# Kernel optimization log

Measured on AMD Instinct MI355X. Metric: run time of the kernel, lower is better.

The kernel has to match this reference:

```python
import jax, jax.numpy as jnp
import numpy as np

B, S, E = 2, 2049, 512
H, WIN = 8, 1024
D = E // H


def setup_inputs() -> dict:
    key = jax.random.key(0)
    ks = jax.random.split(key, 11)
    sc = 0.02
    return {
        "x": jax.random.normal(ks[0], (B, S, E), dtype=jnp.float32),
        "Wq": jax.random.normal(ks[1], (E, E), dtype=jnp.float32) * sc,
        "bq": jnp.zeros((E,), dtype=jnp.float32),
        "Wk": jax.random.normal(ks[2], (E, E), dtype=jnp.float32) * sc,
        "bk": jnp.zeros((E,), dtype=jnp.float32),
        "Wv": jax.random.normal(ks[3], (E, E), dtype=jnp.float32) * sc,
        "bv": jnp.zeros((E,), dtype=jnp.float32),
        "Wo": jax.random.normal(ks[4], (E, E), dtype=jnp.float32) * sc,
        "bo": jnp.zeros((E,), dtype=jnp.float32),
        "w_gate": jax.random.normal(ks[5], (2 * E,), dtype=jnp.float32) * sc,
        "b_gate": jnp.zeros((), dtype=jnp.float32),
    }


def reference(x, Wq, bq, Wk, bk, Wv, bv, Wo, bo, w_gate, b_gate):
    scale = D ** -0.5
    q_flat = x @ Wq + bq  # [B,S,E]
    k_flat = x @ Wk + bk
    v_flat = x @ Wv + bv
    q = q_flat.reshape(B, S, H, D).transpose(0, 2, 1, 3)  # [B,H,S,D]
    k = k_flat.reshape(B, S, H, D).transpose(0, 2, 1, 3)
    v = v_flat.reshape(B, S, H, D).transpose(0, 2, 1, 3)

    scores = jnp.einsum("bhqd,bhkd->bhqk", q, k) * scale  # [B,H,S,S]

    # Gaussian positional bias: -0.5*|i-j|^2/sigma^2, sigma = window/2
    pos = jnp.arange(S)
    dist = jnp.abs(pos[:, None] - pos[None, :]).astype(jnp.float32)
    sigma = WIN / 2.0
    bias = -0.5 * dist ** 2 / (sigma ** 2)  # [S,S]
    scores = scores + bias[None, None]

    # Pairwise gate: sigmoid(concat(q_i,k_j) @ w + b) == sigmoid(q_i.wq + k_j.wk + b)
    gq = q_flat @ w_gate[:E]       # [B,S]
    gk = k_flat @ w_gate[E:]       # [B,S]
    gates = jax.nn.sigmoid(gq[:, :, None] + gk[:, None, :] + b_gate)  # [B,S,S]
    scores = scores * gates[:, None]  # broadcast over heads

    local_mask = jnp.where(dist <= WIN, 0.0, -jnp.inf).astype(jnp.float32)
    scores = scores + local_mask[None, None]

    attn = jax.nn.softmax(scores, axis=-1)
    out = jnp.einsum("bhqk,bhkd->bhqd", attn, v)  # [B,H,S,D]
    out = out.transpose(0, 2, 1, 3).reshape(B, S, E)
    return out @ Wo + bo
```

## Files before the change

### kernel.cpp

```cpp
#include <hip/hip_runtime.h>
#include <cstdint>
#include <cstddef>

#define B_ 2
#define S_ 2049
#define E_ 512
#define H_ 8
#define WIN_ 1024
#define MROWS (B_*S_)
#define SP_ 2176
#define GBUFN 4104
#define BHS_ (B_*H_*S_)

typedef unsigned short ushort_t;
typedef __attribute__((ext_vector_type(8))) short bf16x8;
typedef __attribute__((ext_vector_type(4))) float f32x4;

#define MFMA16(a,b,c) __builtin_amdgcn_mfma_f32_16x16x32_bf16(a,b,c,0,0,0)

__device__ __forceinline__ ushort_t f2bf(float f) {
  unsigned int u = __float_as_uint(f);
  u += 0x7fffu + ((u >> 16) & 1u);
  return (ushort_t)(u >> 16);
}
__device__ __forceinline__ float bf2f(ushort_t h) {
  return __uint_as_float(((unsigned int)h) << 16);
}

__global__ __launch_bounds__(256) void convert_w_kernel(
    const float* __restrict__ W0, const float* __restrict__ W1,
    const float* __restrict__ W2, const float* __restrict__ W3,
    ushort_t* __restrict__ Wt_all, ushort_t* __restrict__ WoHi,
    float* __restrict__ gacc)
{
  __shared__ float tile[32][33];
  int wid = blockIdx.x;
  int z = wid >> 8, rem = wid & 255;
  if (z == 3) {
    int gz = rem * 256 + threadIdx.x;
    if (gz < 2 * GBUFN) gacc[gz] = 0.f;
  }
  const float* W = (z == 0) ? W0 : (z == 1) ? W1 : (z == 2) ? W2 : W3;
  int k0 = (rem >> 4) * 32, n0 = (rem & 15) * 32;
  int r = threadIdx.x >> 5, c = threadIdx.x & 31;
#pragma unroll
  for (int i = 0; i < 4; ++i) {
    int rr = r + i * 8;
    tile[rr][c] = W[(size_t)(k0 + rr) * E_ + n0 + c];
  }
  __syncthreads();
#pragma unroll
  for (int i = 0; i < 4; ++i) {
    int rr = r + i * 8;
    float v = tile[c][rr];
    size_t dst = (size_t)(n0 + rr) * E_ + k0 + c;
    if (z < 3) Wt_all[(size_t)z * E_ * E_ + dst] = f2bf(v);
    else       WoHi[dst] = f2bf(v);
  }
}

__global__ __launch_bounds__(256) void gemm_qkv_kernel(
    const float* __restrict__ x, const ushort_t* __restrict__ Wt_all,
    const float* __restrict__ bq, const float* __restrict__ bk,
    const float* __restrict__ bv, const float* __restrict__ wg,
    ushort_t* __restrict__ qkb, ushort_t* __restrict__ vT,
    float* __restrict__ gacc)
{
  __shared__ __align__(16) ushort_t As[64][72];
  __shared__ __align__(16) ushort_t Bs[128][72];
  int tid = threadIdx.x;
  int lane = tid & 63, w = tid >> 6;
  int l15 = lane & 15, quad = lane >> 4;
  int wm = (w & 1) * 32, wn = (w >> 1) * 64;
  int z = blockIdx.z;
  const ushort_t* Wt = Wt_all + (size_t)z * E_ * E_;
  const float* bias = (z == 0) ? bq : (z == 1) ? bk : bv;
  int bt = blockIdx.x;
  int bg2 = bt / 33;
  int bm = (bt - bg2 * 33) * 64;
  int bn = blockIdx.y * 128;
  size_t rowbase = (size_t)bg2 * S_;

  int ar = tid >> 2, acq = (tid & 3) * 16;
  int ai = bm + ar; if (ai >= S_) ai = S_ - 1;
  const float* ap = x + (size_t)(rowbase + ai) * E_ + acq;
  int br = tid >> 1, bcq = (tid & 1) * 32;
  const ushort_t* bp = Wt + (size_t)(bn + br) * E_ + bcq;

  const f32x4 fz = {0.f, 0.f, 0.f, 0.f};
  f32x4 acc[2][4];
#pragma unroll
  for (int mt = 0; mt < 2; ++mt)
#pragma unroll
    for (int nt = 0; nt < 4; ++nt) acc[mt][nt] = fz;

  float4 pa0 = *(const float4*)ap,        pa1 = *(const float4*)(ap + 4);
  float4 pa2 = *(const float4*)(ap + 8),  pa3 = *(const float4*)(ap + 12);
  int4 pb0 = *(const int4*)bp,        pb1 = *(const int4*)(bp + 8);
  int4 pb2 = *(const int4*)(bp + 16), pb3 = *(const int4*)(bp + 24);

  for (int k0 = 0; k0 < E_; k0 += 64) {
    __syncthreads();
    int kn = (k0 + 64 < E_) ? (k0 + 64) : k0;
    float4 na0 = *(const float4*)(ap + kn),      na1 = *(const float4*)(ap + kn + 4);
    float4 na2 = *(const float4*)(ap + kn + 8),  na3 = *(const float4*)(ap + kn + 12);
    int4 nb0 = *(const int4*)(bp + kn),      nb1 = *(const int4*)(bp + kn + 8);
    int4 nb2 = *(const int4*)(bp + kn + 16), nb3 = *(const int4*)(bp + kn + 24);
    {
      unsigned int c0, c1, c2, c3, c4, c5, c6, c7;
      asm("v_cvt_pk_bf16_f32 %0, %1, %2" : "=v"(c0) : "v"(pa0.x), "v"(pa0.y));
      asm("v_cvt_pk_bf16_f32 %0, %1, %2" : "=v"(c1) : "v"(pa0.z), "v"(pa0.w));
      asm("v_cvt_pk_bf16_f32 %0, %1, %2" : "=v"(c2) : "v"(pa1.x), "v"(pa1.y));
      asm("v_cvt_pk_bf16_f32 %0, %1, %2" : "=v"(c3) : "v"(pa1.z), "v"(pa1.w));
      asm("v_cvt_pk_bf16_f32 %0, %1, %2" : "=v"(c4) : "v"(pa2.x), "v"(pa2.y));
      asm("v_cvt_pk_bf16_f32 %0, %1, %2" : "=v"(c5) : "v"(pa2.z), "v"(pa2.w));
      asm("v_cvt_pk_bf16_f32 %0, %1, %2" : "=v"(c6) : "v"(pa3.x), "v"(pa3.y));
      asm("v_cvt_pk_bf16_f32 %0, %1, %2" : "=v"(c7) : "v"(pa3.z), "v"(pa3.w));
      int4 A0; A0.x = (int)c0; A0.y = (int)c1; A0.z = (int)c2; A0.w = (int)c3;
      int4 A1; A1.x = (int)c4; A1.y = (int)c5; A1.z = (int)c6; A1.w = (int)c7;
      *(int4*)&As[ar][acq] = A0; *(int4*)&As[ar][acq + 8] = A1;
    }
    *(int4*)&Bs[br][bcq] = pb0;      *(int4*)&Bs[br][bcq + 8] = pb1;
    *(int4*)&Bs[br][bcq + 16] = pb2; *(int4*)&Bs[br][bcq + 24] = pb3;
    __syncthreads();
    bf16x8 a[2][2], bfr[4][2];
#pragma unroll
    for (int mt = 0; mt < 2; ++mt) {
      a[mt][0] = *(const bf16x8*)&As[wm + mt * 16 + l15][quad * 8];
      a[mt][1] = *(const bf16x8*)&As[wm + mt * 16 + l15][32 + quad * 8];
    }
#pragma unroll
    for (int nt = 0; nt < 4; ++nt) {
      bfr[nt][0] = *(const bf16x8*)&Bs[wn + nt * 16 + l15][quad * 8];
      bfr[nt][1] = *(const bf16x8*)&Bs[wn + nt * 16 + l15][32 + quad * 8];
    }
    __builtin_amdgcn_s_setprio(1);
#pragma unroll
    for (int mt = 0; mt < 2; ++mt)
#pragma unroll
      for (int nt = 0; nt < 4; ++nt) {
        acc[mt][nt] = MFMA16(a[mt][0], bfr[nt][0], acc[mt][nt]);
        acc[mt][nt] = MFMA16(a[mt][1], bfr[nt][1], acc[mt][nt]);
      }
    __builtin_amdgcn_s_setprio(0);
    pa0 = na0; pa1 = na1; pa2 = na2; pa3 = na3;
    pb0 = nb0; pb1 = nb1; pb2 = nb2; pb3 = nb3;
  }

  float bb[4];
#pragma unroll
  for (int nt = 0; nt < 4; ++nt) bb[nt] = bias[bn + wn + nt * 16 + l15];

  if (z < 2) {
    ushort_t* C = qkb + (size_t)z * MROWS * E_;
#pragma unroll
    for (int mt = 0; mt < 2; ++mt)
#pragma unroll
      for (int nt = 0; nt < 4; ++nt)
#pragma unroll
        for (int r = 0; r < 4; ++r) {
          int i = bm + wm + mt * 16 + quad * 4 + r;
          if (i < S_)
            C[(rowbase + i) * E_ + bn + wn + nt * 16 + l15] = f2bf(acc[mt][nt][r] + bb[nt]);
        }
    const float* wgp = wg + (size_t)z * E_;
    float wv[4];
#pragma unroll
    for (int nt = 0; nt < 4; ++nt) wv[nt] = wgp[bn + wn + nt * 16 + l15];
    float* gp = gacc + (size_t)z * GBUFN;
#pragma unroll
    for (int mt = 0; mt < 2; ++mt)
#pragma unroll
      for (int r = 0; r < 4; ++r) {
        float s = 0.f;
#pragma unroll
        for (int nt = 0; nt < 4; ++nt) s = fmaf(acc[mt][nt][r] + bb[nt], wv[nt], s);
        s += __shfl_xor(s, 1, 16); s += __shfl_xor(s, 2, 16);
        s += __shfl_xor(s, 4, 16); s += __shfl_xor(s, 8, 16);
        int i = bm + wm + mt * 16 + quad * 4 + r;
        if (l15 == 0 && i < S_) atomicAdd(&gp[rowbase + i], s);
      }
  } else {
    ushort_t* lt = &Bs[0][0];
    int ti = tid >> 2, tc = (tid & 3) * 16;
#pragma unroll
    for (int hh = 0; hh < 2; ++hh) {
      __syncthreads();
      if ((w >> 1) == hh) {
#pragma unroll
        for (int mt = 0; mt < 2; ++mt)
#pragma unroll
          for (int nt = 0; nt < 4; ++nt) {
            int d = nt * 16 + l15;
#pragma unroll
            for (int r = 0; r < 4; ++r) {
              int il = wm + mt * 16 + quad * 4 + r;
              lt[d * 72 + il] = f2bf(acc[mt][nt][r] + bb[nt]);
            }
          }
      }
      __syncthreads();
      int hg = (bn >> 6) + hh;
      union { int4 q[2]; ushort_t u[16]; } tv;
      tv.q[0] = *(const int4*)&lt[ti * 72 + tc];
      tv.q[1] = *(const int4*)&lt[ti * 72 + tc + 8];
      size_t vrow = ((size_t)(bg2 * H_ + hg) * 64 + ti) * SP_;
#pragma unroll
      for (int c8 = 0; c8 < 2; ++c8) {
        int i2 = bm + tc + c8 * 8;
        if (i2 + 7 < S_) {
          *(int4*)&vT[vrow + i2] = tv.q[c8];
        } else {
#pragma unroll
          for (int e = 0; e < 8; ++e)
            if (i2 + e < S_) vT[vrow + i2 + e] = tv.u[c8 * 8 + e];
        }
      }
    }
  }
}

__device__ __forceinline__ int swz(int row, int slot) {
  return row * 64 + ((slot ^ (row & 7)) << 3);
}

__global__ __launch_bounds__(256) void attn_kernel(
    const ushort_t* __restrict__ qb, const ushort_t* __restrict__ kb,
    const ushort_t* __restrict__ vT, const float* __restrict__ gq_raw,
    const float* __restrict__ gk_raw, const float* __restrict__ bgate,
    float* __restrict__ Opart, float* __restrict__ Lpart)
{
  __shared__ __align__(16) ushort_t Ks[64 * 64];
  __shared__ __align__(16) ushort_t Vt[64 * 64];
  __shared__ __align__(16) ushort_t Ps[4 * 16 * 64];
  __shared__ float gbs[704];

  int tid = threadIdx.x;
  int lane = tid & 63, w = tid >> 6;
  int l15 = lane & 15, quad = lane >> 4;

  int sub = blockIdx.x % 48;
  int qidx = blockIdx.x / 48;
  int off = (qidx + 1) >> 1;
  int qt = 16 + ((qidx & 1) ? -off : off);
  int bh = sub & 15, third = sub >> 4;
  int h = bh & 7, b = bh >> 3;
  int i0 = qt * 64;
  const float LOG2E = 1.44269504f;
  const float coef2 = (-0.5f / (512.f * 512.f)) * LOG2E;
  const float QSC = 0.125f * LOG2E;

  int i = i0 + w * 16 + l15;
  int ic = (i < S_) ? i : S_ - 1;
  bf16x8 qf0 = *(const bf16x8*)&qb[((size_t)(b * S_ + ic)) * E_ + h * 64 + quad * 8];
  bf16x8 qf1 = *(const bf16x8*)&qb[((size_t)(b * S_ + ic)) * E_ + h * 64 + 32 + quad * 8];
#pragma unroll
  for (int e = 0; e < 8; ++e) {
    qf0[e] = (short)f2bf(bf2f((ushort_t)qf0[e]) * QSC);
    qf1[e] = (short)f2bf(bf2f((ushort_t)qf1[e]) * QSC);
  }
  float av = __expf(-(gq_raw[b * S_ + ic] + bgate[0]));
  float fdi = (i < S_) ? (float)i : -1e5f;

  int jlo = i0 - WIN_; if (jlo < 0) jlo = 0;
  int jt_lo = jlo >> 6;
  int jhi = i0 + 63 + WIN_; if (jhi > S_ - 1) jhi = S_ - 1;
  int jt_hi = jhi >> 6;
  int L = jt_hi - jt_lo + 1;
  int n0 = (L + 2) / 3, n1 = (L + 1) / 3;
  int myLo = jt_lo + ((third == 0) ? 0 : (third == 1) ? n0 : n0 + n1);
  int cnt = (third == 0) ? n0 : (third == 1) ? n1 : L - n0 - n1;
  int myHi = myLo + cnt - 1;
  int jbase = myLo << 6;
  int nwin = cnt << 6;

  for (int tt = tid; tt < nwin; tt += 256) {
    int j = jbase + tt; int jc = (j < S_) ? j : S_ - 1;
    gbs[tt] = __expf(-gk_raw[b * S_ + jc]);
  }

  int srow = tid >> 2, sc4 = tid & 3;
  int scol = sc4 * 16;
  int wl0 = swz(srow, 2 * sc4), wl1 = swz(srow, 2 * sc4 + 1);
  const ushort_t* kb_base = kb + (size_t)b * S_ * E_ + h * 64 + scol;
  const ushort_t* vb_base = vT + ((size_t)(b * H_ + h) * 64 + srow) * SP_ + scol;

  int4 ka0, ka1, va0, va1;
  {
    int jc0 = jbase + srow; if (jc0 > S_ - 1) jc0 = S_ - 1;
    const int4* kp = (const int4*)(kb_base + (size_t)jc0 * E_);
    ka0 = kp[0]; ka1 = kp[1];
    const int4* vp = (const int4*)(vb_base + jbase);
    va0 = vp[0]; va1 = vp[1];
  }

  const f32x4 fz = {0.f, 0.f, 0.f, 0.f};
  f32x4 Ov[4] = {fz, fz, fz, fz};
  const bf16x8 ones = {16256, 16256, 16256, 16256, 16256, 16256, 16256, 16256};
  f32x4 Lv = fz;

  int psb = w * 1024;
  int pw[4];
#pragma unroll
  for (int nt = 0; nt < 4; ++nt)
    pw[nt] = psb + l15 * 64 + (((2 * nt + (quad >> 1)) ^ (l15 & 7)) << 3) + (quad & 1) * 4;
  int pr0 = psb + swz(l15, quad), pr1 = psb + swz(l15, 4 + quad);

  for (int jt = myLo; jt <= myHi; ++jt) {
    int j0 = jt << 6;
    __syncthreads();
    int jn = (jt < myHi) ? ((jt + 1) << 6) : j0;
    int jcn = jn + srow; if (jcn > S_ - 1) jcn = S_ - 1;
    const int4* kp = (const int4*)(kb_base + (size_t)jcn * E_);
    int4 nk0 = kp[0], nk1 = kp[1];
    const int4* vp = (const int4*)(vb_base + jn);
    int4 nv0 = vp[0], nv1 = vp[1];
    *(int4*)&Ks[wl0] = ka0; *(int4*)&Ks[wl1] = ka1;
    *(int4*)&Vt[wl0] = va0; *(int4*)&Vt[wl1] = va1;
    __syncthreads();

    f32x4 st[4];
    __builtin_amdgcn_s_setprio(1);
#pragma unroll
    for (int nt = 0; nt < 4; ++nt) {
      int Rk = nt * 16 + l15;
      bf16x8 kf0 = *(const bf16x8*)&Ks[swz(Rk, quad)];
      bf16x8 kf1 = *(const bf16x8*)&Ks[swz(Rk, 4 + quad)];
      f32x4 s = MFMA16(kf0, qf0, fz);
      st[nt] = MFMA16(kf1, qf1, s);
    }
    __builtin_amdgcn_s_setprio(0);

    bool full = ((j0 + 63 - i0) <= WIN_) && ((i0 + 63 - j0) <= WIN_)
                && (j0 + 63 < S_) && (i0 + 63 < S_);
    float fq = fdi - (float)(j0 + quad * 4);
    if (full) {
#pragma unroll
      for (int nt = 0; nt < 4; ++nt) {
        f32x4 g4 = *(const f32x4*)&gbs[(j0 - jbase) + nt * 16 + quad * 4];
#pragma unroll
        for (int r = 0; r < 4; ++r) {
          float f = fq - (float)(nt * 16 + r);
          float gate = __builtin_amdgcn_rcpf(fmaf(av, g4[r], 1.f));
          float p = __builtin_amdgcn_exp2f(fmaf(f * f, coef2, st[nt][r]) * gate);
          st[nt][r] = p;
        }
      }
    } else {
#pragma unroll
      for (int nt = 0; nt < 4; ++nt) {
        f32x4 g4 = *(const f32x4*)&gbs[(j0 - jbase) + nt * 16 + quad * 4];
#pragma unroll
        for (int r = 0; r < 4; ++r) {
          int j = j0 + nt * 16 + quad * 4 + r;
          float fj = (j < S_) ? (float)j : 1e5f;
          float f = fdi - fj;
          float gate = __builtin_amdgcn_rcpf(fmaf(av, g4[r], 1.f));
          float t = fmaf(f * f, coef2, st[nt][r]) * gate;
          t = (__builtin_fabsf(f) <= 1024.f) ? t : -1e30f;
          float p = __builtin_amdgcn_exp2f(t);
          st[nt][r] = p;
        }
      }
    }

#pragma unroll
    for (int nt = 0; nt < 4; ++nt) {
      unsigned int k0p, k1p;
      asm("v_cvt_pk_bf16_f32 %0, %1, %2" : "=v"(k0p) : "v"(st[nt][0]), "v"(st[nt][1]));
      asm("v_cvt_pk_bf16_f32 %0, %1, %2" : "=v"(k1p) : "v"(st[nt][2]), "v"(st[nt][3]));
      uint2 pk; pk.x = k0p; pk.y = k1p;
      *(uint2*)&Ps[pw[nt]] = pk;
    }
    bf16x8 p0 = *(const bf16x8*)&Ps[pr0];
    bf16x8 p1 = *(const bf16x8*)&Ps[pr1];
    __builtin_amdgcn_s_setprio(1);
#pragma unroll
    for (int nt = 0; nt < 4; ++nt) {
      int Rv = nt * 16 + l15;
      bf16x8 v0 = *(const bf16x8*)&Vt[swz(Rv, quad)];
      bf16x8 v1 = *(const bf16x8*)&Vt[swz(Rv, 4 + quad)];
      Ov[nt] = MFMA16(p0, v0, Ov[nt]);
      Ov[nt] = MFMA16(p1, v1, Ov[nt]);
    }
    Lv = MFMA16(p0, ones, Lv);
    Lv = MFMA16(p1, ones, Lv);
    __builtin_amdgcn_s_setprio(0);
    ka0 = nk0; ka1 = nk1; va0 = nv0; va1 = nv1;
  }

#pragma unroll
  for (int r = 0; r < 4; ++r) {
    int irow = i0 + w * 16 + quad * 4 + r;
    if (l15 == 0 && irow < S_)
      Lpart[(size_t)third * BHS_ + (size_t)(b * H_ + h) * S_ + irow] = Lv[r];
  }
#pragma unroll
  for (int r = 0; r < 4; ++r) {
    int irow = i0 + w * 16 + quad * 4 + r;
    if (irow < S_) {
      size_t base = ((size_t)third * BHS_ + (size_t)(b * H_ + h) * S_ + irow) * 64;
#pragma unroll
      for (int nt = 0; nt < 4; ++nt)
        Opart[base + nt * 16 + l15] = Ov[nt][r];
    }
  }
}

__global__ __launch_bounds__(256) void combine_kernel(
    const float* __restrict__ Opart, const float* __restrict__ Lpart,
    ushort_t* __restrict__ ahi, ushort_t* __restrict__ alo)
{
  int tid = threadIdx.x;
  int gi = blockIdx.x * 16 + (tid >> 4);
  int d4 = tid & 15;
  int b = gi / (H_ * S_);
  int rem = gi - b * (H_ * S_);
  int h = rem / S_;
  int i = rem - h * S_;
  size_t p0 = (size_t)(b * H_ + h) * S_ + i;
  float l = Lpart[p0] + Lpart[p0 + (size_t)BHS_] + Lpart[p0 + 2 * (size_t)BHS_];
  float inv = 1.f / l;
  const float* op = Opart + p0 * 64 + d4 * 4;
  float4 o1 = *(const float4*)op;
  float4 o2 = *(const float4*)(op + (size_t)BHS_ * 64);
  float4 o3 = *(const float4*)(op + 2 * (size_t)BHS_ * 64);
  float o[4] = {(o1.x + o2.x + o3.x) * inv, (o1.y + o2.y + o3.y) * inv,
                (o1.z + o2.z + o3.z) * inv, (o1.w + o2.w + o3.w) * inv};
  ushort4 hi, lo;
  hi.x = f2bf(o[0]); lo.x = f2bf(o[0] - bf2f(hi.x));
  hi.y = f2bf(o[1]); lo.y = f2bf(o[1] - bf2f(hi.y));
  hi.z = f2bf(o[2]); lo.z = f2bf(o[2] - bf2f(hi.z));
  hi.w = f2bf(o[3]); lo.w = f2bf(o[3] - bf2f(hi.w));
  size_t oidx = ((size_t)b * S_ + i) * E_ + h * 64 + d4 * 4;
  *(ushort4*)&ahi[oidx] = hi;
  *(ushort4*)&alo[oidx] = lo;
}

__global__ __launch_bounds__(256) void gemm_out_kernel(
    const ushort_t* __restrict__ Ahi, const ushort_t* __restrict__ Alo,
    const ushort_t* __restrict__ Whi, const float* __restrict__ bias,
    float* __restrict__ C)
{
  __shared__ __align__(16) ushort_t AsH[64][72];
  __shared__ __align__(16) ushort_t AsL[64][72];
  __shared__ __align__(16) ushort_t BsW[64][72];
  int tid = threadIdx.x;
  int lane = tid & 63, w = tid >> 6;
  int l15 = lane & 15, quad = lane >> 4;
  int wm = (w & 1) * 32, wn = (w >> 1) * 32;
  int bm = blockIdx.x * 64, bn = blockIdx.y * 64;

  int sr = tid >> 2, sc = (tid & 3) * 16;
  int am = bm + sr; if (am >= MROWS) am = MROWS - 1;
  const ushort_t* ahp = Ahi + (size_t)am * E_ + sc;
  const ushort_t* alp = Alo + (size_t)am * E_ + sc;
  const ushort_t* bp = Whi + (size_t)(bn + sr) * E_ + sc;

  const f32x4 fz = {0.f, 0.f, 0.f, 0.f};
  f32x4 acc[2][2];
#pragma unroll
  for (int mt = 0; mt < 2; ++mt)
#pragma unroll
    for (int nt = 0; nt < 2; ++nt) acc[mt][nt] = fz;

  int4 ph0 = *(const int4*)ahp, ph1 = *(const int4*)(ahp + 8);
  int4 pl0 = *(const int4*)alp, pl1 = *(const int4*)(alp + 8);
  int4 pb0 = *(const int4*)bp,  pb1 = *(const int4*)(bp + 8);

  for (int k0 = 0; k0 < E_; k0 += 64) {
    __syncthreads();
    int kn = (k0 + 64 < E_) ? (k0 + 64) : k0;
    int4 nh0 = *(const int4*)(ahp + kn), nh1 = *(const int4*)(ahp + kn + 8);
    int4 nl0 = *(const int4*)(alp + kn), nl1 = *(const int4*)(alp + kn + 8);
    int4 nb0 = *(const int4*)(bp + kn),  nb1 = *(const int4*)(bp + kn + 8);
    *(int4*)&AsH[sr][sc] = ph0; *(int4*)&AsH[sr][sc + 8] = ph1;
    *(int4*)&AsL[sr][sc] = pl0; *(int4*)&AsL[sr][sc + 8] = pl1;
    *(int4*)&BsW[sr][sc] = pb0; *(int4*)&BsW[sr][sc + 8] = pb1;
    __syncthreads();
    bf16x8 ah[2][2], al[2][2], bw[2][2];
#pragma unroll
    for (int mt = 0; mt < 2; ++mt) {
      ah[mt][0] = *(const bf16x8*)&AsH[wm + mt * 16 + l15][quad * 8];
      ah[mt][1] = *(const bf16x8*)&AsH[wm + mt * 16 + l15][32 + quad * 8];
      al[mt][0] = *(const bf16x8*)&AsL[wm + mt * 16 + l15][quad * 8];
      al[mt][1] = *(const bf16x8*)&AsL[wm + mt * 16 + l15][32 + quad * 8];
    }
#pragma unroll
    for (int nt = 0; nt < 2; ++nt) {
      bw[nt][0] = *(const bf16x8*)&BsW[wn + nt * 16 + l15][quad * 8];
      bw[nt][1] = *(const bf16x8*)&BsW[wn + nt * 16 + l15][32 + quad * 8];
    }
    __builtin_amdgcn_s_setprio(1);
#pragma unroll
    for (int mt = 0; mt < 2; ++mt)
#pragma unroll
      for (int nt = 0; nt < 2; ++nt) {
        acc[mt][nt] = MFMA16(ah[mt][0], bw[nt][0], acc[mt][nt]);
        acc[mt][nt] = MFMA16(al[mt][0], bw[nt][0], acc[mt][nt]);
        acc[mt][nt] = MFMA16(ah[mt][1], bw[nt][1], acc[mt][nt]);
        acc[mt][nt] = MFMA16(al[mt][1], bw[nt][1], acc[mt][nt]);
      }
    __builtin_amdgcn_s_setprio(0);
    ph0 = nh0; ph1 = nh1; pl0 = nl0; pl1 = nl1; pb0 = nb0; pb1 = nb1;
  }
#pragma unroll
  for (int nt = 0; nt < 2; ++nt) {
    float bb = bias[bn + wn + nt * 16 + l15];
#pragma unroll
    for (int mt = 0; mt < 2; ++mt)
#pragma unroll
      for (int r = 0; r < 4; ++r) {
        int m = bm + wm + mt * 16 + quad * 4 + r;
        if (m < MROWS)
          C[(size_t)m * E_ + bn + wn + nt * 16 + l15] = acc[mt][nt][r] + bb;
      }
  }
}

extern "C" void kernel_launch(void* const* d_in, const int* in_sizes, int n_in,
                              void* d_out, int out_size, void* d_ws, size_t ws_size,
                              hipStream_t stream) {
  const float* x  = (const float*)d_in[0];
  const float* Wq = (const float*)d_in[1];
  const float* bq = (const float*)d_in[2];
  const float* Wk = (const float*)d_in[3];
  const float* bk = (const float*)d_in[4];
  const float* Wv = (const float*)d_in[5];
  const float* bv = (const float*)d_in[6];
  const float* Wo = (const float*)d_in[7];
  const float* bo = (const float*)d_in[8];
  const float* wg = (const float*)d_in[9];
  const float* bg = (const float*)d_in[10];

  char* p = (char*)d_ws;
  ushort_t* Wt_all = (ushort_t*)p; p += (size_t)3 * E_ * E_ * 2;
  ushort_t* WoHi   = (ushort_t*)p; p += (size_t)E_ * E_ * 2;
  ushort_t* qkb    = (ushort_t*)p; p += (size_t)2 * MROWS * E_ * 2;
  ushort_t* vT     = (ushort_t*)p; p += (size_t)B_ * H_ * 64 * SP_ * 2;
  float*    gacc   = (float*)p;    p += (size_t)2 * GBUFN * 4;
  float*    Opart  = (float*)p;    p += (size_t)3 * BHS_ * 64 * 4;
  float*    Lpart  = (float*)p;    p += (size_t)3 * BHS_ * 4;
  ushort_t* aHi    = qkb;
  ushort_t* aLo    = qkb + (size_t)MROWS * E_;

  hipLaunchKernelGGL(convert_w_kernel, dim3(1024), dim3(256), 0, stream,
                     Wq, Wk, Wv, Wo, Wt_all, WoHi, gacc);
  hipLaunchKernelGGL(gemm_qkv_kernel, dim3(66, 4, 3), dim3(256), 0, stream,
                     x, Wt_all, bq, bk, bv, wg, qkb, vT, gacc);
  hipLaunchKernelGGL(attn_kernel, dim3(33 * 48), dim3(256), 0, stream,
                     qkb, qkb + (size_t)MROWS * E_, vT, gacc, gacc + GBUFN, bg,
                     Opart, Lpart);
  hipLaunchKernelGGL(combine_kernel, dim3(2049), dim3(256), 0, stream,
                     Opart, Lpart, aHi, aLo);
  hipLaunchKernelGGL(gemm_out_kernel, dim3(65, 8), dim3(256), 0, stream,
                     aHi, aLo, WoHi, bo, (float*)d_out);
}
```

Measured before the change: 160.1 us.

## Fuse split-softmax combine into output projection GEMM A-tile loads

Removes the separate combine kernel and has the output GEMM read the three partial attention outputs and normalizers directly, summing, normalizing and splitting into bf16 hi/lo while staging A tiles. It also uses packed bf16 conversion instructions. This removes a launch and the intermediate hi/lo activation buffers. In exchange, each of the 8 column blocks re-reads and re-reduces the fp32 partials, which greatly increases global/L2 traffic.

```diff
diff --git a/kernel.cpp b/kernel.cpp
--- a/kernel.cpp
+++ b/kernel.cpp
@@ -407,38 +407,8 @@
   }
 }
 
-__global__ __launch_bounds__(256) void combine_kernel(
+__global__ __launch_bounds__(256) void gemm_out_kernel(
     const float* __restrict__ Opart, const float* __restrict__ Lpart,
-    ushort_t* __restrict__ ahi, ushort_t* __restrict__ alo)
-{
-  int tid = threadIdx.x;
-  int gi = blockIdx.x * 16 + (tid >> 4);
-  int d4 = tid & 15;
-  int b = gi / (H_ * S_);
-  int rem = gi - b * (H_ * S_);
-  int h = rem / S_;
-  int i = rem - h * S_;
-  size_t p0 = (size_t)(b * H_ + h) * S_ + i;
-  float l = Lpart[p0] + Lpart[p0 + (size_t)BHS_] + Lpart[p0 + 2 * (size_t)BHS_];
-  float inv = 1.f / l;
-  const float* op = Opart + p0 * 64 + d4 * 4;
-  float4 o1 = *(const float4*)op;
-  float4 o2 = *(const float4*)(op + (size_t)BHS_ * 64);
-  float4 o3 = *(const float4*)(op + 2 * (size_t)BHS_ * 64);
-  float o[4] = {(o1.x + o2.x + o3.x) * inv, (o1.y + o2.y + o3.y) * inv,
-                (o1.z + o2.z + o3.z) * inv, (o1.w + o2.w + o3.w) * inv};
-  ushort4 hi, lo;
-  hi.x = f2bf(o[0]); lo.x = f2bf(o[0] - bf2f(hi.x));
-  hi.y = f2bf(o[1]); lo.y = f2bf(o[1] - bf2f(hi.y));
-  hi.z = f2bf(o[2]); lo.z = f2bf(o[2] - bf2f(hi.z));
-  hi.w = f2bf(o[3]); lo.w = f2bf(o[3] - bf2f(hi.w));
-  size_t oidx = ((size_t)b * S_ + i) * E_ + h * 64 + d4 * 4;
-  *(ushort4*)&ahi[oidx] = hi;
-  *(ushort4*)&alo[oidx] = lo;
-}
-
-__global__ __launch_bounds__(256) void gemm_out_kernel(
-    const ushort_t* __restrict__ Ahi, const ushort_t* __restrict__ Alo,
     const ushort_t* __restrict__ Whi, const float* __restrict__ bias,
     float* __restrict__ C)
 {
@@ -453,8 +423,9 @@
 
   int sr = tid >> 2, sc = (tid & 3) * 16;
   int am = bm + sr; if (am >= MROWS) am = MROWS - 1;
-  const ushort_t* ahp = Ahi + (size_t)am * E_ + sc;
-  const ushort_t* alp = Alo + (size_t)am * E_ + sc;
+  int ab = (am >= S_) ? 1 : 0;
+  int ai = am - ab * S_;
+  size_t rb = (size_t)(ab * H_) * S_ + ai;
   const ushort_t* bp = Whi + (size_t)(bn + sr) * E_ + sc;
 
   const f32x4 fz = {0.f, 0.f, 0.f, 0.f};
@@ -464,18 +435,76 @@
 #pragma unroll
     for (int nt = 0; nt < 2; ++nt) acc[mt][nt] = fz;
 
-  int4 ph0 = *(const int4*)ahp, ph1 = *(const int4*)(ahp + 8);
-  int4 pl0 = *(const int4*)alp, pl1 = *(const int4*)(alp + 8);
+  float4 pa[4]; float pinv;
+  {
+    int kk = sc;
+    int hh = kk >> 6, dd = kk & 63;
+    size_t ro = rb + (size_t)hh * S_;
+    const float* p0 = Opart + ro * 64 + dd;
+    const float* p1 = p0 + (size_t)BHS_ * 64;
+    const float* p2 = p1 + (size_t)BHS_ * 64;
+#pragma unroll
+    for (int t = 0; t < 4; ++t) {
+      float4 a = *(const float4*)(p0 + t * 4);
+      float4 b = *(const float4*)(p1 + t * 4);
+      float4 c = *(const float4*)(p2 + t * 4);
+      pa[t].x = a.x + b.x + c.x; pa[t].y = a.y + b.y + c.y;
+      pa[t].z = a.z + b.z + c.z; pa[t].w = a.w + b.w + c.w;
+    }
+    float lsum = Lpart[ro] + Lpart[ro + (size_t)BHS_] + Lpart[ro + 2 * (size_t)BHS_];
+    pinv = 1.f / lsum;
+  }
   int4 pb0 = *(const int4*)bp,  pb1 = *(const int4*)(bp + 8);
 
   for (int k0 = 0; k0 < E_; k0 += 64) {
     __syncthreads();
     int kn = (k0 + 64 < E_) ? (k0 + 64) : k0;
-    int4 nh0 = *(const int4*)(ahp + kn), nh1 = *(const int4*)(ahp + kn + 8);
-    int4 nl0 = *(const int4*)(alp + kn), nl1 = *(const int4*)(alp + kn + 8);
+    float4 na[4]; float ninv;
+    {
+      int kk = kn + sc;
+      int hh = kk >> 6, dd = kk & 63;
+      size_t ro = rb + (size_t)hh * S_;
+      const float* p0 = Opart + ro * 64 + dd;
+      const float* p1 = p0 + (size_t)BHS_ * 64;
+      const float* p2 = p1 + (size_t)BHS_ * 64;
+#pragma unroll
+      for (int t = 0; t < 4; ++t) {
+        float4 a = *(const float4*)(p0 + t * 4);
+        float4 b = *(const float4*)(p1 + t * 4);
+        float4 c = *(const float4*)(p2 + t * 4);
+        na[t].x = a.x + b.x + c.x; na[t].y = a.y + b.y + c.y;
+        na[t].z = a.z + b.z + c.z; na[t].w = a.w + b.w + c.w;
+      }
+      float lsum = Lpart[ro] + Lpart[ro + (size_t)BHS_] + Lpart[ro + 2 * (size_t)BHS_];
+      ninv = 1.f / lsum;
+    }
     int4 nb0 = *(const int4*)(bp + kn),  nb1 = *(const int4*)(bp + kn + 8);
-    *(int4*)&AsH[sr][sc] = ph0; *(int4*)&AsH[sr][sc + 8] = ph1;
-    *(int4*)&AsL[sr][sc] = pl0; *(int4*)&AsL[sr][sc + 8] = pl1;
+
+    {
+      float oe[16] = {pa[0].x, pa[0].y, pa[0].z, pa[0].w,
+                      pa[1].x, pa[1].y, pa[1].z, pa[1].w,
+                      pa[2].x, pa[2].y, pa[2].z, pa[2].w,
+                      pa[3].x, pa[3].y, pa[3].z, pa[3].w};
+      unsigned int hw[8], lw[8];
+#pragma unroll
+      for (int pq = 0; pq < 8; ++pq) {
+        float o0 = oe[2 * pq] * pinv, o1 = oe[2 * pq + 1] * pinv;
+        unsigned int hp;
+        asm("v_cvt_pk_bf16_f32 %0, %1, %2" : "=v"(hp) : "v"(o0), "v"(o1));
+        float h0 = __uint_as_float(hp << 16);
+        float h1 = __uint_as_float(hp & 0xffff0000u);
+        unsigned int lp;
+        float l0 = o0 - h0, l1 = o1 - h1;
+        asm("v_cvt_pk_bf16_f32 %0, %1, %2" : "=v"(lp) : "v"(l0), "v"(l1));
+        hw[pq] = hp; lw[pq] = lp;
+      }
+      int4 H0; H0.x = (int)hw[0]; H0.y = (int)hw[1]; H0.z = (int)hw[2]; H0.w = (int)hw[3];
+      int4 H1; H1.x = (int)hw[4]; H1.y = (int)hw[5]; H1.z = (int)hw[6]; H1.w = (int)hw[7];
+      int4 L0; L0.x = (int)lw[0]; L0.y = (int)lw[1]; L0.z = (int)lw[2]; L0.w = (int)lw[3];
+      int4 L1; L1.x = (int)lw[4]; L1.y = (int)lw[5]; L1.z = (int)lw[6]; L1.w = (int)lw[7];
+      *(int4*)&AsH[sr][sc] = H0; *(int4*)&AsH[sr][sc + 8] = H1;
+      *(int4*)&AsL[sr][sc] = L0; *(int4*)&AsL[sr][sc + 8] = L1;
+    }
     *(int4*)&BsW[sr][sc] = pb0; *(int4*)&BsW[sr][sc + 8] = pb1;
     __syncthreads();
     bf16x8 ah[2][2], al[2][2], bw[2][2];
@@ -502,7 +531,8 @@
         acc[mt][nt] = MFMA16(al[mt][1], bw[nt][1], acc[mt][nt]);
       }
     __builtin_amdgcn_s_setprio(0);
-    ph0 = nh0; ph1 = nh1; pl0 = nl0; pl1 = nl1; pb0 = nb0; pb1 = nb1;
+    pa[0] = na[0]; pa[1] = na[1]; pa[2] = na[2]; pa[3] = na[3]; pinv = ninv;
+    pb0 = nb0; pb1 = nb1;
   }
 #pragma unroll
   for (int nt = 0; nt < 2; ++nt) {
@@ -541,8 +571,6 @@
   float*    gacc   = (float*)p;    p += (size_t)2 * GBUFN * 4;
   float*    Opart  = (float*)p;    p += (size_t)3 * BHS_ * 64 * 4;
   float*    Lpart  = (float*)p;    p += (size_t)3 * BHS_ * 4;
-  ushort_t* aHi    = qkb;
-  ushort_t* aLo    = qkb + (size_t)MROWS * E_;
 
   hipLaunchKernelGGL(convert_w_kernel, dim3(1024), dim3(256), 0, stream,
                      Wq, Wk, Wv, Wo, Wt_all, WoHi, gacc);
@@ -551,8 +579,6 @@
   hipLaunchKernelGGL(attn_kernel, dim3(33 * 48), dim3(256), 0, stream,
                      qkb, qkb + (size_t)MROWS * E_, vT, gacc, gacc + GBUFN, bg,
                      Opart, Lpart);
-  hipLaunchKernelGGL(combine_kernel, dim3(2049), dim3(256), 0, stream,
-                     Opart, Lpart, aHi, aLo);
   hipLaunchKernelGGL(gemm_out_kernel, dim3(65, 8), dim3(256), 0, stream,
-                     aHi, aLo, WoHi, bo, (float*)d_out);
-}
+                     Opart, Lpart, WoHi, bo, (float*)d_out);
+}
```

After: 177.5 us. 10.9% more time.

## Fuse split-KV combine into attention kernel via last-arriver atomic counter

Applied to the files above, without the earlier changes.

Removes the separate combine kernel. Each attention block now increments a per-(query tile, head) atomic counter after writing its partial O and L, and the third block to arrive reads the other two partials, normalises, and writes the bf16 hi/lo attention output directly. This saves a kernel launch and avoids re-reading its own partial from global memory. In exchange it adds a thread fence and an atomic per block, plus a serial tail for the last arriver. The aHi/aLo buffers move to a dedicated workspace region, because q/k are still being read while the outputs are written.

```diff
diff --git a/kernel.cpp b/kernel.cpp
--- a/kernel.cpp
+++ b/kernel.cpp
@@ -11,6 +11,7 @@
 #define SP_ 2176
 #define GBUFN 4104
 #define BHS_ (B_*H_*S_)
+#define NCNT 528
 
 typedef unsigned short ushort_t;
 typedef __attribute__((ext_vector_type(8))) short bf16x8;
@@ -31,7 +32,7 @@
     const float* __restrict__ W0, const float* __restrict__ W1,
     const float* __restrict__ W2, const float* __restrict__ W3,
     ushort_t* __restrict__ Wt_all, ushort_t* __restrict__ WoHi,
-    float* __restrict__ gacc)
+    float* __restrict__ gacc, unsigned int* __restrict__ cnt)
 {
   __shared__ float tile[32][33];
   int wid = blockIdx.x;
@@ -39,6 +40,7 @@
   if (z == 3) {
     int gz = rem * 256 + threadIdx.x;
     if (gz < 2 * GBUFN) gacc[gz] = 0.f;
+    if (gz < NCNT) cnt[gz] = 0u;
   }
   const float* W = (z == 0) ? W0 : (z == 1) ? W1 : (z == 2) ? W2 : W3;
   int k0 = (rem >> 4) * 32, n0 = (rem & 15) * 32;
@@ -228,12 +230,15 @@
     const ushort_t* __restrict__ qb, const ushort_t* __restrict__ kb,
     const ushort_t* __restrict__ vT, const float* __restrict__ gq_raw,
     const float* __restrict__ gk_raw, const float* __restrict__ bgate,
-    float* __restrict__ Opart, float* __restrict__ Lpart)
+    float* __restrict__ Opart, float* __restrict__ Lpart,
+    unsigned int* __restrict__ cnt, ushort_t* __restrict__ ahi,
+    ushort_t* __restrict__ alo)
 {
   __shared__ __align__(16) ushort_t Ks[64 * 64];
   __shared__ __align__(16) ushort_t Vt[64 * 64];
   __shared__ __align__(16) ushort_t Ps[4 * 16 * 64];
   __shared__ float gbs[704];
+  __shared__ int sOld;
 
   int tid = threadIdx.x;
   int lane = tid & 63, w = tid >> 6;
@@ -269,10 +274,10 @@
   int L = jt_hi - jt_lo + 1;
   int n0 = (L + 2) / 3, n1 = (L + 1) / 3;
   int myLo = jt_lo + ((third == 0) ? 0 : (third == 1) ? n0 : n0 + n1);
-  int cnt = (third == 0) ? n0 : (third == 1) ? n1 : L - n0 - n1;
-  int myHi = myLo + cnt - 1;
+  int cntJ = (third == 0) ? n0 : (third == 1) ? n1 : L - n0 - n1;
+  int myHi = myLo + cntJ - 1;
   int jbase = myLo << 6;
-  int nwin = cnt << 6;
+  int nwin = cntJ << 6;
 
   for (int tt = tid; tt < nwin; tt += 256) {
     int j = jbase + tt; int jc = (j < S_) ? j : S_ - 1;
@@ -405,36 +410,35 @@
         Opart[base + nt * 16 + l15] = Ov[nt][r];
     }
   }
-}
-
-__global__ __launch_bounds__(256) void combine_kernel(
-    const float* __restrict__ Opart, const float* __restrict__ Lpart,
-    ushort_t* __restrict__ ahi, ushort_t* __restrict__ alo)
-{
-  int tid = threadIdx.x;
-  int gi = blockIdx.x * 16 + (tid >> 4);
-  int d4 = tid & 15;
-  int b = gi / (H_ * S_);
-  int rem = gi - b * (H_ * S_);
-  int h = rem / S_;
-  int i = rem - h * S_;
-  size_t p0 = (size_t)(b * H_ + h) * S_ + i;
-  float l = Lpart[p0] + Lpart[p0 + (size_t)BHS_] + Lpart[p0 + 2 * (size_t)BHS_];
-  float inv = 1.f / l;
-  const float* op = Opart + p0 * 64 + d4 * 4;
-  float4 o1 = *(const float4*)op;
-  float4 o2 = *(const float4*)(op + (size_t)BHS_ * 64);
-  float4 o3 = *(const float4*)(op + 2 * (size_t)BHS_ * 64);
-  float o[4] = {(o1.x + o2.x + o3.x) * inv, (o1.y + o2.y + o3.y) * inv,
-                (o1.z + o2.z + o3.z) * inv, (o1.w + o2.w + o3.w) * inv};
-  ushort4 hi, lo;
-  hi.x = f2bf(o[0]); lo.x = f2bf(o[0] - bf2f(hi.x));
-  hi.y = f2bf(o[1]); lo.y = f2bf(o[1] - bf2f(hi.y));
-  hi.z = f2bf(o[2]); lo.z = f2bf(o[2] - bf2f(hi.z));
-  hi.w = f2bf(o[3]); lo.w = f2bf(o[3] - bf2f(hi.w));
-  size_t oidx = ((size_t)b * S_ + i) * E_ + h * 64 + d4 * 4;
-  *(ushort4*)&ahi[oidx] = hi;
-  *(ushort4*)&alo[oidx] = lo;
+
+  __threadfence();
+  __syncthreads();
+  if (tid == 0) sOld = (int)atomicAdd(&cnt[qt * 16 + bh], 1u);
+  __syncthreads();
+  if (sOld == 2) {
+    __threadfence();
+    int ta = (third + 1) % 3, tb = (third + 2) % 3;
+#pragma unroll
+    for (int r = 0; r < 4; ++r) {
+      int irow = i0 + w * 16 + quad * 4 + r;
+      if (irow < S_) {
+        size_t ro = (size_t)(b * H_ + h) * S_ + irow;
+        float l = Lv[r] + Lpart[(size_t)ta * BHS_ + ro] + Lpart[(size_t)tb * BHS_ + ro];
+        float inv = 1.f / l;
+        size_t ba = ((size_t)ta * BHS_ + ro) * 64;
+        size_t bb2 = ((size_t)tb * BHS_ + ro) * 64;
+        size_t oidx = ((size_t)b * S_ + irow) * E_ + h * 64;
+#pragma unroll
+        for (int nt = 0; nt < 4; ++nt) {
+          int c = nt * 16 + l15;
+          float o = (Ov[nt][r] + Opart[ba + c] + Opart[bb2 + c]) * inv;
+          ushort_t hi = f2bf(o);
+          ahi[oidx + c] = hi;
+          alo[oidx + c] = f2bf(o - bf2f(hi));
+        }
+      }
+    }
+  }
 }
 
 __global__ __launch_bounds__(256) void gemm_out_kernel(
@@ -539,20 +543,19 @@
   ushort_t* qkb    = (ushort_t*)p; p += (size_t)2 * MROWS * E_ * 2;
   ushort_t* vT     = (ushort_t*)p; p += (size_t)B_ * H_ * 64 * SP_ * 2;
   float*    gacc   = (float*)p;    p += (size_t)2 * GBUFN * 4;
+  unsigned int* cnt = (unsigned int*)p; p += (size_t)NCNT * 4;
   float*    Opart  = (float*)p;    p += (size_t)3 * BHS_ * 64 * 4;
   float*    Lpart  = (float*)p;    p += (size_t)3 * BHS_ * 4;
-  ushort_t* aHi    = qkb;
-  ushort_t* aLo    = qkb + (size_t)MROWS * E_;
+  ushort_t* aHi    = (ushort_t*)p; p += (size_t)MROWS * E_ * 2;
+  ushort_t* aLo    = (ushort_t*)p; p += (size_t)MROWS * E_ * 2;
 
   hipLaunchKernelGGL(convert_w_kernel, dim3(1024), dim3(256), 0, stream,
-                     Wq, Wk, Wv, Wo, Wt_all, WoHi, gacc);
+                     Wq, Wk, Wv, Wo, Wt_all, WoHi, gacc, cnt);
   hipLaunchKernelGGL(gemm_qkv_kernel, dim3(66, 4, 3), dim3(256), 0, stream,
                      x, Wt_all, bq, bk, bv, wg, qkb, vT, gacc);
   hipLaunchKernelGGL(attn_kernel, dim3(33 * 48), dim3(256), 0, stream,
                      qkb, qkb + (size_t)MROWS * E_, vT, gacc, gacc + GBUFN, bg,
-                     Opart, Lpart);
-  hipLaunchKernelGGL(combine_kernel, dim3(2049), dim3(256), 0, stream,
-                     Opart, Lpart, aHi, aLo);
+                     Opart, Lpart, cnt, aHi, aLo);
   hipLaunchKernelGGL(gemm_out_kernel, dim3(65, 8), dim3(256), 0, stream,
                      aHi, aLo, WoHi, bo, (float*)d_out);
 }
```

New measurement: 417.6 us. 2.61x slower.
